# Optimization experiments

Measured on AMD Instinct MI355X. Metric: run time of the kernel, lower is better.

The kernel has to match this reference:

```python
import jax, jax.numpy as jnp
import numpy as np

B, C, H, W = 32, 128, 128, 128
K = 32  # num_codes


def setup_inputs() -> dict:
    key = jax.random.key(0)
    k1, k2, k3 = jax.random.split(key, 3)
    std = 1.0 / (K * C) ** 0.5
    x = jax.random.normal(k1, (B, C, H, W), dtype=jnp.float32)
    codewords = jax.random.uniform(k2, (K, C), dtype=jnp.float32, minval=-std, maxval=std)
    scale = jax.random.uniform(k3, (K,), dtype=jnp.float32, minval=-1.0, maxval=0.0)
    return {"x": x, "codewords": codewords, "scale": scale}


def reference(x, codewords, scale):
    b, c, h, w = x.shape
    # [b, N, C] with N = H*W
    xf = jnp.transpose(x.reshape(b, c, h * w), (0, 2, 1))
    # scaled L2 distances without materializing [b,N,K,C]:
    x2 = jnp.sum(xf * xf, axis=-1, keepdims=True)          # [b, N, 1]
    c2 = jnp.sum(codewords * codewords, axis=-1)           # [K]
    xc = jnp.einsum('bnc,kc->bnk', xf, codewords)          # [b, N, K]
    dist = x2 - 2.0 * xc + c2[None, None, :]               # [b, N, K]
    scaled = scale[None, None, :] * dist                   # [b, N, K]
    aw = jax.nn.softmax(scaled, axis=2)                    # [b, N, K]
    # aggregate: sum_n aw[b,n,k] * (x[b,n,c] - codewords[k,c])
    wx = jnp.einsum('bnk,bnc->bkc', aw, xf)                # [b, K, C]
    wsum = jnp.sum(aw, axis=1)                             # [b, K]
    encoded = wx - wsum[:, :, None] * codewords[None, :, :]
    return encoded  # [b, K, C]
```

## Files before the change

### kernel.cpp

```cpp
#include <hip/hip_runtime.h>

#define N_SP 16384
#define C_DIM 128
#define K_DIM 32
#define TILEN 32
#define NBP   128

typedef short short8 __attribute__((ext_vector_type(8)));
typedef float f32x16 __attribute__((ext_vector_type(16)));

__device__ __forceinline__ unsigned f2bfu(float f){
    return (__float_as_uint(f) + 0x8000u) >> 16;
}
__device__ __forceinline__ unsigned short f2bf(float f){
    return (unsigned short)f2bfu(f);
}
__device__ __forceinline__ float bf2f(unsigned u){
    return __uint_as_float(u << 16);
}

#define SWZ(row, n) (((row) << 5) + ((n) ^ (((row) & 3) << 3)))

union FragU { int i[4]; short8 s; };

__global__ __launch_bounds__(64) void enc_main(
    const float* __restrict__ x,
    const float* __restrict__ cw,
    const float* __restrict__ scale,
    unsigned short* __restrict__ wxp,
    float* __restrict__ wsp)
{
    __shared__ unsigned short xs[C_DIM * TILEN];
    __shared__ unsigned short aws[K_DIM * TILEN];
    const int t   = threadIdx.x;
    const int r   = blockIdx.x;
    const int b   = blockIdx.y;
    const int hi  = t >> 5;
    const int l31 = t & 31;

    const int nbase = r * 128;

    const float* xb = x + (size_t)b * C_DIM * N_SP + (size_t)(hi * 64) * N_SP;

    const float s_k = scale[l31];
    const float m2s = -2.f * s_k;
    float c2p = 0.f;
    short8 cwA[8];
#pragma unroll
    for (int ksg = 0; ksg < 8; ++ksg){
        const float* cp = cw + l31 * C_DIM + ksg * 16 + hi * 8;
        float4 a  = *(const float4*)cp;
        float4 b4 = *(const float4*)(cp + 4);
        c2p = fmaf(a.x, a.x, c2p);  c2p = fmaf(a.y, a.y, c2p);
        c2p = fmaf(a.z, a.z, c2p);  c2p = fmaf(a.w, a.w, c2p);
        c2p = fmaf(b4.x, b4.x, c2p); c2p = fmaf(b4.y, b4.y, c2p);
        c2p = fmaf(b4.z, b4.z, c2p); c2p = fmaf(b4.w, b4.w, c2p);
        FragU f;
        f.i[0] = (int)(f2bfu(m2s * a.x)  | (f2bfu(m2s * a.y)  << 16));
        f.i[1] = (int)(f2bfu(m2s * a.z)  | (f2bfu(m2s * a.w)  << 16));
        f.i[2] = (int)(f2bfu(m2s * b4.x) | (f2bfu(m2s * b4.y) << 16));
        f.i[3] = (int)(f2bfu(m2s * b4.z) | (f2bfu(m2s * b4.w) << 16));
        cwA[ksg] = f.s;
    }
    const float c2 = c2p + __shfl_xor(c2p, 32);

    {
        float* combof = (float*)aws;
        combof[2 * l31]     = s_k;
        combof[2 * l31 + 1] = s_k * c2;
    }
    float csx[16], csy[16];
#pragma unroll
    for (int q = 0; q < 16; ++q){
        const int row = (q & 3) + 8 * (q >> 2) + 4 * hi;
        const float* combof = (const float*)aws;
        csx[q] = combof[2 * row];
        csy[q] = combof[2 * row + 1];
    }

    f32x16 acc0, acc1, acc2, acc3, accS;
#pragma unroll
    for (int i = 0; i < 16; ++i){
        acc0[i]=0.f; acc1[i]=0.f; acc2[i]=0.f; acc3[i]=0.f; accS[i]=0.f;
    }
    short8 ones;
#pragma unroll
    for (int i = 0; i < 8; ++i) ones[i] = (short)0x3F80;

#pragma unroll 1
    for (int tile = 0; tile < 4; ++tile){
        const int n0 = nbase + tile * TILEN;
        const float* xp = xb + n0 + l31;

        __syncthreads();

        f32x16 sA;
#pragma unroll
        for (int i = 0; i < 16; ++i) sA[i] = 0.f;

        float x2 = 0.f;
        int xr[32];

        float cur[8], nx1[8];
#pragma unroll
        for (int j = 0; j < 8; ++j) cur[j] = xp[(size_t)j * N_SP];
#pragma unroll
        for (int j = 0; j < 8; ++j) nx1[j] = xp[(size_t)(8 + j) * N_SP];

#pragma unroll
        for (int g = 0; g < 8; ++g){
            float nx2[8];
            if (g < 6){
#pragma unroll
                for (int j = 0; j < 8; ++j) nx2[j] = xp[(size_t)((g + 2) * 8 + j) * N_SP];
            } else {
#pragma unroll
                for (int j = 0; j < 8; ++j) nx2[j] = 0.f;
            }
#pragma unroll
            for (int j = 0; j < 8; j += 2){
                const int rl = g * 8 + j;
                const int c  = hi * 64 + rl;
                const float a0 = cur[j], a1 = cur[j + 1];
                x2 = fmaf(a0, a0, x2);
                x2 = fmaf(a1, a1, x2);
                const unsigned u0 = f2bfu(a0), u1 = f2bfu(a1);
                xs[SWZ(c,     l31)] = (unsigned short)u0;
                xs[SWZ(c + 1, l31)] = (unsigned short)u1;
                xr[rl >> 1] = (int)(u0 | (u1 << 16));
            }
            if (g < 7){
#pragma unroll
                for (int j = 0; j < 8; ++j){ cur[j] = nx1[j]; nx1[j] = nx2[j]; }
            }
        }

#pragma unroll
        for (int ks = 0; ks < 8; ++ks){
            FragU f;
            if (ks < 4){
#pragma unroll
                for (int d = 0; d < 4; ++d){
                    const int own = xr[ks * 8 + d];
                    const int oth = __shfl_xor(xr[ks * 8 + 4 + d], 32);
                    f.i[d] = hi ? oth : own;
                }
            } else {
                const int k4 = ks - 4;
#pragma unroll
                for (int d = 0; d < 4; ++d){
                    const int own = xr[k4 * 8 + 4 + d];
                    const int oth = __shfl_xor(xr[k4 * 8 + d], 32);
                    f.i[d] = hi ? own : oth;
                }
            }
            sA = __builtin_amdgcn_mfma_f32_32x32x16_bf16(cwA[ks], f.s, sA, 0, 0, 0);
        }

        const float x2f = x2 + __shfl_xor(x2, 32);
        {
            float arg[16]; float ml = -3.4e38f;
#pragma unroll
            for (int q = 0; q < 16; ++q){
                arg[q] = fmaf(csx[q], x2f, sA[q] + csy[q]);
                ml = fmaxf(ml, arg[q]);
            }
            const float mm = fmaxf(ml, __shfl_xor(ml, 32));
            float sum = 0.f;
#pragma unroll
            for (int q = 0; q < 16; ++q){ float p = __expf(arg[q] - mm); arg[q] = p; sum += p; }
            sum += __shfl_xor(sum, 32);
            const float rr = 1.f / sum;
#pragma unroll
            for (int q = 0; q < 16; ++q){
                const int row = (q & 3) + 8 * (q >> 2) + 4 * hi;
                aws[SWZ(row, l31)] = f2bf(arg[q] * rr);
            }
        }

        __syncthreads();

#pragma unroll
        for (int ks = 0; ks < 2; ++ks){
            const int n8 = ks * 16 + hi * 8;
            short8 af  = *(const short8*)(const void*)&aws[SWZ(l31, n8)];
            short8 bf0 = *(const short8*)(const void*)&xs[SWZ(l31,      n8)];
            short8 bf1 = *(const short8*)(const void*)&xs[SWZ(32 + l31, n8)];
            short8 bf2 = *(const short8*)(const void*)&xs[SWZ(64 + l31, n8)];
            short8 bf3 = *(const short8*)(const void*)&xs[SWZ(96 + l31, n8)];
            acc0 = __builtin_amdgcn_mfma_f32_32x32x16_bf16(af, bf0, acc0, 0, 0, 0);
            acc1 = __builtin_amdgcn_mfma_f32_32x32x16_bf16(af, bf1, acc1, 0, 0, 0);
            acc2 = __builtin_amdgcn_mfma_f32_32x32x16_bf16(af, bf2, acc2, 0, 0, 0);
            acc3 = __builtin_amdgcn_mfma_f32_32x32x16_bf16(af, bf3, acc3, 0, 0, 0);
            accS = __builtin_amdgcn_mfma_f32_32x32x16_bf16(af, ones, accS, 0, 0, 0);
        }
    }

    const int blk = b * NBP + r;
    unsigned short* wxp_blk = wxp + (size_t)blk * (K_DIM * C_DIM);
#pragma unroll
    for (int rg = 0; rg < 16; ++rg){
        const int row = (rg & 3) + 8 * (rg >> 2) + 4 * hi;
        wxp_blk[row * C_DIM +      l31] = f2bf(acc0[rg]);
        wxp_blk[row * C_DIM + 32 + l31] = f2bf(acc1[rg]);
        wxp_blk[row * C_DIM + 64 + l31] = f2bf(acc2[rg]);
        wxp_blk[row * C_DIM + 96 + l31] = f2bf(acc3[rg]);
    }
    if (l31 == 0){
        float* wsp_blk = wsp + (size_t)blk * K_DIM;
#pragma unroll
        for (int rg = 0; rg < 16; ++rg){
            const int row = (rg & 3) + 8 * (rg >> 2) + 4 * hi;
            wsp_blk[row] = accS[rg];
        }
    }
}

__global__ __launch_bounds__(256) void enc_reduce(
    const unsigned short* __restrict__ wxp, const float* __restrict__ wsp,
    const float* __restrict__ cw, float* __restrict__ out)
{
    const int t = threadIdx.x;
    const int k = blockIdx.x & (K_DIM - 1);
    const int b = blockIdx.x >> 5;

    __shared__ float ps[8][C_DIM];
    __shared__ float wsl[4];

    float wv = (t < NBP) ? wsp[(size_t)(b * NBP + t) * K_DIM + k] : 0.f;
#pragma unroll
    for (int off = 32; off; off >>= 1) wv += __shfl_down(wv, off);
    if ((t & 63) == 0) wsl[t >> 6] = wv;

    const int c4 = (t & 31) * 4;
    const int jg = t >> 5;
    float4 s; s.x = 0.f; s.y = 0.f; s.z = 0.f; s.w = 0.f;
    const unsigned short* pp = wxp + ((size_t)(b * NBP) + jg) * (K_DIM * C_DIM) + k * C_DIM + c4;
#pragma unroll
    for (int j = 0; j < NBP; j += 8){
        uint2 v = *(const uint2*)(pp + (size_t)j * (K_DIM * C_DIM));
        s.x += bf2f(v.x & 0xFFFFu);
        s.y += bf2f(v.x >> 16);
        s.z += bf2f(v.y & 0xFFFFu);
        s.w += bf2f(v.y >> 16);
    }
    *(float4*)&ps[jg][c4] = s;
    __syncthreads();

    if (t < C_DIM){
        const float wsh = wsl[0] + wsl[1];
        float rsum = 0.f;
#pragma unroll
        for (int j2 = 0; j2 < 8; ++j2) rsum += ps[j2][t];
        out[((size_t)b * K_DIM + k) * C_DIM + t] = rsum - wsh * cw[k * C_DIM + t];
    }
}

extern "C" void kernel_launch(void* const* d_in, const int* in_sizes, int n_in,
                              void* d_out, int out_size, void* d_ws, size_t ws_size,
                              hipStream_t stream){
    (void)in_sizes; (void)n_in; (void)out_size; (void)ws_size;
    const float* x     = (const float*)d_in[0];
    const float* cw    = (const float*)d_in[1];
    const float* scale = (const float*)d_in[2];
    float* out = (float*)d_out;

    char* p = (char*)d_ws;
    unsigned short* wxp = (unsigned short*)p;
    p += (size_t)32 * NBP * K_DIM * C_DIM * sizeof(unsigned short);
    float* wsp = (float*)p;

    enc_main<<<dim3(NBP, 32), 64, 0, stream>>>(x, cw, scale, wxp, wsp);
    enc_reduce<<<32 * K_DIM, 256, 0, stream>>>(wxp, wsp, cw, out);
}
```

Measured before the change: 69.38 us.

## Use two waves per block and reduce partials in LDS before writeback

Each block now runs two wavefronts, each covering its own 128-position slice with private LDS tiles. Their accumulators are summed through shared memory before a single bf16 partial write, which halves the number of partial blocks (NBP 128 to 64). This cuts partial-sum write traffic and the work of the reduce kernel. In exchange it adds LDS use and block-level barriers, and the block count drops, which may lower occupancy.

```diff
diff --git a/kernel.cpp b/kernel.cpp
--- a/kernel.cpp
+++ b/kernel.cpp
@@ -4,7 +4,7 @@
 #define C_DIM 128
 #define K_DIM 32
 #define TILEN 32
-#define NBP   128
+#define NBP   64
 
 typedef short short8 __attribute__((ext_vector_type(8)));
 typedef float f32x16 __attribute__((ext_vector_type(16)));
@@ -23,22 +23,27 @@
 
 union FragU { int i[4]; short8 s; };
 
-__global__ __launch_bounds__(64) void enc_main(
+__global__ __launch_bounds__(128) void enc_main(
     const float* __restrict__ x,
     const float* __restrict__ cw,
     const float* __restrict__ scale,
     unsigned short* __restrict__ wxp,
     float* __restrict__ wsp)
 {
-    __shared__ unsigned short xs[C_DIM * TILEN];
-    __shared__ unsigned short aws[K_DIM * TILEN];
+    __shared__ unsigned short sh[2 * (C_DIM + K_DIM) * TILEN];
+
     const int t   = threadIdx.x;
+    const int w   = t >> 6;
+    const int l   = t & 63;
     const int r   = blockIdx.x;
     const int b   = blockIdx.y;
-    const int hi  = t >> 5;
+    const int hi  = (t >> 5) & 1;
     const int l31 = t & 31;
 
-    const int nbase = r * 128;
+    unsigned short* xs  = sh + w * ((C_DIM + K_DIM) * TILEN);
+    unsigned short* aws = xs + C_DIM * TILEN;
+
+    const int nbase = r * 256 + w * 128;
 
     const float* xb = x + (size_t)b * C_DIM * N_SP + (size_t)(hi * 64) * N_SP;
 
@@ -196,22 +201,41 @@
         }
     }
 
-    const int blk = b * NBP + r;
-    unsigned short* wxp_blk = wxp + (size_t)blk * (K_DIM * C_DIM);
-#pragma unroll
-    for (int rg = 0; rg < 16; ++rg){
-        const int row = (rg & 3) + 8 * (rg >> 2) + 4 * hi;
-        wxp_blk[row * C_DIM +      l31] = f2bf(acc0[rg]);
-        wxp_blk[row * C_DIM + 32 + l31] = f2bf(acc1[rg]);
-        wxp_blk[row * C_DIM + 64 + l31] = f2bf(acc2[rg]);
-        wxp_blk[row * C_DIM + 96 + l31] = f2bf(acc3[rg]);
-    }
-    if (l31 == 0){
-        float* wsp_blk = wsp + (size_t)blk * K_DIM;
+    __syncthreads();
+    float* fbuf = (float*)sh;
+    if (w == 1){
 #pragma unroll
         for (int rg = 0; rg < 16; ++rg){
+            fbuf[(0 * 16 + rg) * 64 + l] = acc0[rg];
+            fbuf[(1 * 16 + rg) * 64 + l] = acc1[rg];
+            fbuf[(2 * 16 + rg) * 64 + l] = acc2[rg];
+            fbuf[(3 * 16 + rg) * 64 + l] = acc3[rg];
+            fbuf[(4 * 16 + rg) * 64 + l] = accS[rg];
+        }
+    }
+    __syncthreads();
+    if (w == 0){
+        const int blk = b * NBP + r;
+        unsigned short* wxp_blk = wxp + (size_t)blk * (K_DIM * C_DIM);
+#pragma unroll
+        for (int rg = 0; rg < 16; ++rg){
+            const float a0 = acc0[rg] + fbuf[(0 * 16 + rg) * 64 + l];
+            const float a1 = acc1[rg] + fbuf[(1 * 16 + rg) * 64 + l];
+            const float a2 = acc2[rg] + fbuf[(2 * 16 + rg) * 64 + l];
+            const float a3 = acc3[rg] + fbuf[(3 * 16 + rg) * 64 + l];
             const int row = (rg & 3) + 8 * (rg >> 2) + 4 * hi;
-            wsp_blk[row] = accS[rg];
+            wxp_blk[row * C_DIM +      l31] = f2bf(a0);
+            wxp_blk[row * C_DIM + 32 + l31] = f2bf(a1);
+            wxp_blk[row * C_DIM + 64 + l31] = f2bf(a2);
+            wxp_blk[row * C_DIM + 96 + l31] = f2bf(a3);
+        }
+        if (l31 == 0){
+            float* wsp_blk = wsp + (size_t)blk * K_DIM;
+#pragma unroll
+            for (int rg = 0; rg < 16; ++rg){
+                const int row = (rg & 3) + 8 * (rg >> 2) + 4 * hi;
+                wsp_blk[row] = accS[rg] + fbuf[(4 * 16 + rg) * 64 + l];
+            }
         }
     }
 }
@@ -225,12 +249,14 @@
     const int b = blockIdx.x >> 5;
 
     __shared__ float ps[8][C_DIM];
-    __shared__ float wsl[4];
-
-    float wv = (t < NBP) ? wsp[(size_t)(b * NBP + t) * K_DIM + k] : 0.f;
-#pragma unroll
-    for (int off = 32; off; off >>= 1) wv += __shfl_down(wv, off);
-    if ((t & 63) == 0) wsl[t >> 6] = wv;
+    __shared__ float wsl;
+
+    if (t < 64){
+        float wv = wsp[(size_t)(b * NBP + t) * K_DIM + k];
+#pragma unroll
+        for (int off = 32; off; off >>= 1) wv += __shfl_down(wv, off);
+        if (t == 0) wsl = wv;
+    }
 
     const int c4 = (t & 31) * 4;
     const int jg = t >> 5;
@@ -248,11 +274,10 @@
     __syncthreads();
 
     if (t < C_DIM){
-        const float wsh = wsl[0] + wsl[1];
         float rsum = 0.f;
 #pragma unroll
         for (int j2 = 0; j2 < 8; ++j2) rsum += ps[j2][t];
-        out[((size_t)b * K_DIM + k) * C_DIM + t] = rsum - wsh * cw[k * C_DIM + t];
+        out[((size_t)b * K_DIM + k) * C_DIM + t] = rsum - wsl * cw[k * C_DIM + t];
     }
 }
 
@@ -270,6 +295,6 @@
     p += (size_t)32 * NBP * K_DIM * C_DIM * sizeof(unsigned short);
     float* wsp = (float*)p;
 
-    enc_main<<<dim3(NBP, 32), 64, 0, stream>>>(x, cw, scale, wxp, wsp);
+    enc_main<<<dim3(NBP, 32), 128, 0, stream>>>(x, cw, scale, wxp, wsp);
     enc_reduce<<<32 * K_DIM, 256, 0, stream>>>(wxp, wsp, cw, out);
 }
```

Result: slower. 71.57 us (+3.2%).
